# Optimization experiments

Hardware: AMD Instinct MI355X
Metric: run time of the kernel (lower is better)

Reference implementation:

```python
import jax, jax.numpy as jnp
import numpy as np

H = 32        # num_attention_heads
KV = 8        # num_key_value_heads
D = 128       # head_dim
THETA = 10000.0


def _rope_sincos(seq_len):
    half = D // 2
    i = jnp.arange(half, dtype=jnp.float32)
    # NOTE: original uses theta ** (+2*(i//2)/half) (growing frequencies, not inverse)
    emb = THETA ** (2.0 * jnp.floor(i / 2.0) / half)
    pos = jnp.arange(seq_len, dtype=jnp.float32)
    freqs = pos[:, None] * emb[None, :]            # (S, half)
    sin = jnp.concatenate([jnp.sin(freqs), jnp.sin(freqs)], axis=-1)  # (S, D)
    cos = jnp.concatenate([jnp.cos(freqs), jnp.cos(freqs)], axis=-1)  # (S, D)
    return sin, cos


def _rotate_half(x):
    half = D // 2
    return jnp.concatenate([-x[..., half:], x[..., :half]], axis=-1)


def setup_inputs() -> dict:
    key = jax.random.key(0)
    ks = jax.random.split(key, 5)
    B, S, HS = 2, 4096, 4096
    KVD = KV * D
    return {
        "hidden_states": jax.random.normal(ks[0], (B, S, HS), dtype=jnp.float32) * 0.02,
        "Wq": jax.random.normal(ks[1], (HS, HS), dtype=jnp.float32) * 0.02,
        "Wk": jax.random.normal(ks[2], (HS, KVD), dtype=jnp.float32) * 0.02,
        "Wv": jax.random.normal(ks[3], (HS, KVD), dtype=jnp.float32) * 0.02,
        "Wo": jax.random.normal(ks[4], (HS, HS), dtype=jnp.float32) * 0.02,
    }


def reference(hidden_states, Wq, Wk, Wv, Wo):
    B, S, HS = hidden_states.shape
    q = (hidden_states @ Wq).reshape(B, S, H, D)
    k = (hidden_states @ Wk).reshape(B, S, KV, D)
    v = (hidden_states @ Wv).reshape(B, S, KV, D)

    sin, cos = _rope_sincos(S)
    cos_b = cos[None, :, None, :]  # (1, S, 1, D)
    sin_b = sin[None, :, None, :]
    q = q * cos_b + _rotate_half(q) * sin_b
    k = k * cos_b + _rotate_half(k) * sin_b

    rep = H // KV
    k = jnp.repeat(k, rep, axis=2)  # (B, S, H, D)
    v = jnp.repeat(v, rep, axis=2)

    scale = jnp.sqrt(jnp.float32(D))
    # Faithful to original: matmul batches over (B, S) -> per-position head-head attention
    scores = jnp.einsum('bshd,bstd->bsht', q, k) / scale  # (B, S, H, H)
    attn = jax.nn.softmax(scores, axis=-1)
    out = jnp.einsum('bsht,bstd->bshd', attn, v).reshape(B, S, HS)
    return out @ Wo
```

## Files before the change

### kernel.cpp

```cpp
#include <hip/hip_runtime.h>
#include <cmath>

typedef short short8 __attribute__((ext_vector_type(8)));
typedef float floatx4 __attribute__((ext_vector_type(4)));
typedef unsigned short ushortx4 __attribute__((ext_vector_type(4)));

__device__ inline float bf2f(unsigned short u) {
  return __uint_as_float(((unsigned)u) << 16);
}
__device__ inline unsigned short f2bf(float x) {
  unsigned u = __float_as_uint(x);
  u = (u + 0x7FFFu + ((u >> 16) & 1u)) >> 16;
  return (unsigned short)u;
}

__global__ void probe_kernel(const unsigned short* __restrict__ in, int* __restrict__ flag) {
  __shared__ float red[256];
  float m = 0.f;
  for (int i = threadIdx.x; i < 8192; i += 256) {
    float v = fabsf(bf2f(in[i]));
    if (!isnan(v)) m = fmaxf(m, v);
  }
  red[threadIdx.x] = m;
  __syncthreads();
  for (int s = 128; s > 0; s >>= 1) {
    if (threadIdx.x < s) red[threadIdx.x] = fmaxf(red[threadIdx.x], red[threadIdx.x + s]);
    __syncthreads();
  }
  if (threadIdx.x == 0) flag[0] = (red[0] < 1000.0f) ? 1 : 0;
}

__global__ __launch_bounds__(256) void cast_any(const void* __restrict__ in,
                                                unsigned short* __restrict__ out,
                                                const int* __restrict__ flag, int n) {
  int i = (blockIdx.x * 256 + threadIdx.x) * 4;
  if (i >= n) return;
  if (flag[0]) {
    *(ushortx4*)(out + i) = *(const ushortx4*)((const unsigned short*)in + i);
  } else {
    const float* f = (const float*)in + i;
    ushortx4 o;
    o.x = f2bf(f[0]); o.y = f2bf(f[1]); o.z = f2bf(f[2]); o.w = f2bf(f[3]);
    *(ushortx4*)(out + i) = o;
  }
}

__global__ __launch_bounds__(256) void transpose_cast(const void* __restrict__ W,
                                                      unsigned short* __restrict__ WT,
                                                      const int* __restrict__ flag,
                                                      int N, int rowOff) {
  __shared__ unsigned short tile[32][33];
  int n0 = blockIdx.x * 32, k0 = blockIdx.y * 32;
  int tx = threadIdx.x & 31, ty = threadIdx.x >> 5;
  bool isbf = flag[0] != 0;
#pragma unroll
  for (int p = 0; p < 4; ++p) {
    int k = k0 + ty + p * 8;
    size_t idx = (size_t)k * N + n0 + tx;
    unsigned short b = isbf ? ((const unsigned short*)W)[idx] : f2bf(((const float*)W)[idx]);
    tile[ty + p * 8][tx] = b;
  }
  __syncthreads();
#pragma unroll
  for (int p = 0; p < 4; ++p) {
    int n = n0 + ty + p * 8;
    WT[(size_t)(rowOff + n) * 4096 + k0 + tx] = tile[tx][ty + p * 8];
  }
}

__device__ inline void gload16(const unsigned short* g, unsigned short* lds) {
  __builtin_amdgcn_global_load_lds(
      (const __attribute__((address_space(1))) unsigned int*)g,
      (__attribute__((address_space(3))) unsigned int*)lds, 16, 0, 0);
}

template <int OUTMODE>
__global__ __launch_bounds__(512, 2) void gemm256(const unsigned short* __restrict__ A,
                                                  const unsigned short* __restrict__ BT,
                                                  void* __restrict__ C, int M, int N, int K,
                                                  int nbn, const int* __restrict__ flag) {
  __shared__ __attribute__((aligned(16))) unsigned short As[3][256 * 32];
  __shared__ __attribute__((aligned(16))) unsigned short Bs[3][256 * 32];
  int tid = threadIdx.x;
  int w = tid >> 6, l = tid & 63;
  int wm = w >> 2, wn = w & 3;

  int nwg = gridDim.x;
  int cpx = nwg >> 3;
  int bid = blockIdx.x;
  int swz = (bid & 7) * cpx + (bid >> 3);
  int bm = swz / nbn, bn = swz - bm * nbn;
  int m0 = bm * 256, n0 = bn * 256;

  int sr = tid >> 2;
  int sc = tid & 3;
  int sf = (sr >> 1) & 3;
  int scs = (sc ^ sf) * 8;
  const unsigned short* Ab = A + (size_t)(m0 + sr) * K + scs;
  const unsigned short* Bb = BT + (size_t)(n0 + sr) * K + scs;

  int lane15 = l & 15, q = l >> 4;
  int fl = (lane15 >> 1) & 3;
  int rswz = (q ^ fl) * 8;
  int aoff = (wm * 128 + lane15) * 32 + rswz;
  int boff = (wn * 64 + lane15) * 32 + rswz;

  floatx4 acc[8][4] = {};
  int NT = K >> 5;

  auto stage_half = [&](int tt, int b, int p) {
    gload16(Ab + (size_t)p * 128 * K + (size_t)tt * 32, &As[b][(p * 128 + w * 16) * 32]);
    gload16(Bb + (size_t)p * 128 * K + (size_t)tt * 32, &Bs[b][(p * 128 + w * 16) * 32]);
  };

  stage_half(0, 0, 0);
  stage_half(0, 0, 1);
  stage_half(1, 1, 0);
  stage_half(1, 1, 1);

  int cur = 0;
  for (int t = 0; t < NT; ++t) {
    int nxt2 = cur + 2;
    if (nxt2 >= 3) nxt2 -= 3;
    bool pf = (t + 2 < NT);
    if (t < NT - 1) asm volatile("s_waitcnt vmcnt(4)" ::: "memory");
    else            asm volatile("s_waitcnt vmcnt(0)" ::: "memory");
    __builtin_amdgcn_s_barrier();

    const unsigned short* pA = &As[cur][0];
    const unsigned short* pB = &Bs[cur][0];

    short8 bfr[4], af[4];
#pragma unroll
    for (int i = 0; i < 4; ++i) bfr[i] = *(const short8*)(pB + boff + i * 512);
#pragma unroll
    for (int i = 0; i < 4; ++i) af[i] = *(const short8*)(pA + aoff + i * 512);
    if (pf) stage_half(t + 2, nxt2, 0);
    __builtin_amdgcn_s_barrier();
    __builtin_amdgcn_s_setprio(1);
#pragma unroll
    for (int mi = 0; mi < 4; ++mi)
#pragma unroll
      for (int ni = 0; ni < 4; ++ni)
        acc[mi][ni] = __builtin_amdgcn_mfma_f32_16x16x32_bf16(af[mi], bfr[ni], acc[mi][ni], 0, 0, 0);
    __builtin_amdgcn_s_setprio(0);
    __builtin_amdgcn_s_barrier();

#pragma unroll
    for (int i = 0; i < 4; ++i) af[i] = *(const short8*)(pA + aoff + 2048 + i * 512);
    if (pf) stage_half(t + 2, nxt2, 1);
    __builtin_amdgcn_s_barrier();
    __builtin_amdgcn_s_setprio(1);
#pragma unroll
    for (int mi = 0; mi < 4; ++mi)
#pragma unroll
      for (int ni = 0; ni < 4; ++ni)
        acc[mi + 4][ni] = __builtin_amdgcn_mfma_f32_16x16x32_bf16(af[mi], bfr[ni], acc[mi + 4][ni], 0, 0, 0);
    __builtin_amdgcn_s_setprio(0);

    cur = (cur == 2) ? 0 : cur + 1;
  }

  bool obf = true;
  if (OUTMODE == 1) obf = (flag[0] != 0);
#pragma unroll
  for (int mi = 0; mi < 8; ++mi) {
    int rbase = m0 + wm * 128 + mi * 16 + q * 4;
#pragma unroll
    for (int ni = 0; ni < 4; ++ni) {
      int col = n0 + wn * 64 + ni * 16 + lane15;
#pragma unroll
      for (int rr = 0; rr < 4; ++rr) {
        float v = acc[mi][ni][rr];
        size_t idx = (size_t)(rbase + rr) * N + col;
        if (OUTMODE == 0 || obf)
          ((unsigned short*)C)[idx] = f2bf(v);
        else
          ((float*)C)[idx] = v;
      }
    }
  }
}

__global__ __launch_bounds__(256) void attn_kernel(const unsigned short* __restrict__ QKV,
                                                   unsigned short* __restrict__ AO) {
  __shared__ __attribute__((aligned(16))) float qr[32 * 136];
  __shared__ __attribute__((aligned(16))) float kr[8 * 136];
  __shared__ __attribute__((aligned(16))) float vv[8 * 136];
  __shared__ float P[256];
  __shared__ float sn[64], cs[64];
  int r = blockIdx.x;
  int pos = r & 4095;
  int t = threadIdx.x;
  const unsigned short* row = QKV + (size_t)r * 6144;

  if (t < 64) {
    double e = pow(10000.0, (double)(2 * (t >> 1)) / 64.0);
    float f = (float)pos * (float)e;
    float s_, c_;
    sincosf(f, &s_, &c_);
    sn[t] = s_;
    cs[t] = c_;
  }
  __syncthreads();

#pragma unroll
  for (int p = 0; p < 4; ++p) {
    int e = t + p * 256;
    int head = e >> 7, d = e & 127;
    float x = bf2f(row[4096 + e]);
    float xp = bf2f(row[4096 + (e ^ 64)]);
    float sg = (d < 64) ? -1.f : 1.f;
    kr[head * 136 + d] = x * cs[d & 63] + sg * xp * sn[d & 63];
    vv[head * 136 + d] = bf2f(row[5120 + e]);
  }
#pragma unroll
  for (int p = 0; p < 16; ++p) {
    int e = t + p * 256;
    int head = e >> 7, d = e & 127;
    float x = bf2f(row[e]);
    float xp = bf2f(row[e ^ 64]);
    float sg = (d < 64) ? -1.f : 1.f;
    qr[head * 136 + d] = x * cs[d & 63] + sg * xp * sn[d & 63];
  }
  __syncthreads();

  int h = t >> 3, j = t & 7;
  const float4* q4 = (const float4*)(qr + h * 136);
  const float4* k4 = (const float4*)(kr + j * 136);
  float s = 0.f;
#pragma unroll
  for (int d4 = 0; d4 < 32; ++d4) {
    float4 a = q4[d4], b = k4[d4];
    s += a.x * b.x + a.y * b.y + a.z * b.z + a.w * b.w;
  }
  s *= 0.08838834764831845f;
  float mx = s;
  mx = fmaxf(mx, __shfl_xor(mx, 1));
  mx = fmaxf(mx, __shfl_xor(mx, 2));
  mx = fmaxf(mx, __shfl_xor(mx, 4));
  float ex = expf(s - mx);
  float sm = ex;
  sm += __shfl_xor(sm, 1);
  sm += __shfl_xor(sm, 2);
  sm += __shfl_xor(sm, 4);
  P[t] = ex / sm;
  __syncthreads();

  int d0 = (t & 7) * 16;
  float o[16];
#pragma unroll
  for (int c = 0; c < 16; ++c) o[c] = 0.f;
#pragma unroll
  for (int j2 = 0; j2 < 8; ++j2) {
    float pj = P[h * 8 + j2];
    const float4* v4 = (const float4*)(vv + j2 * 136 + d0);
#pragma unroll
    for (int c = 0; c < 4; ++c) {
      float4 x = v4[c];
      o[c * 4 + 0] += pj * x.x;
      o[c * 4 + 1] += pj * x.y;
      o[c * 4 + 2] += pj * x.z;
      o[c * 4 + 3] += pj * x.w;
    }
  }
  unsigned short* outp = AO + (size_t)r * 4096 + h * 128 + d0;
#pragma unroll
  for (int c = 0; c < 4; ++c) {
    ushortx4 ov;
    ov.x = f2bf(o[c * 4 + 0]);
    ov.y = f2bf(o[c * 4 + 1]);
    ov.z = f2bf(o[c * 4 + 2]);
    ov.w = f2bf(o[c * 4 + 3]);
    *(ushortx4*)(outp + c * 4) = ov;
  }
}

extern "C" void kernel_launch(void* const* d_in, const int* in_sizes, int n_in,
                              void* d_out, int out_size, void* d_ws, size_t ws_size,
                              hipStream_t stream) {
  (void)in_sizes; (void)n_in; (void)out_size; (void)ws_size;
  const void* X  = d_in[0];
  const void* Wq = d_in[1];
  const void* Wk = d_in[2];
  const void* Wv = d_in[3];
  const void* Wo = d_in[4];
  char* ws = (char*)d_ws;
  unsigned short* Xb   = (unsigned short*)(ws);
  unsigned short* WT   = (unsigned short*)(ws + 67108864);
  unsigned short* WoT  = (unsigned short*)(ws + 117440512);
  unsigned short* QKVb = (unsigned short*)(ws + 150994944);
  int* flag            = (int*)(ws + 251658240);
  unsigned short* AO = Xb;

  probe_kernel<<<1, 256, 0, stream>>>((const unsigned short*)X, flag);
  cast_any<<<32768, 256, 0, stream>>>(X, Xb, flag, 33554432);
  transpose_cast<<<dim3(128, 128), 256, 0, stream>>>(Wq, WT, flag, 4096, 0);
  transpose_cast<<<dim3(32, 128), 256, 0, stream>>>(Wk, WT, flag, 1024, 4096);
  transpose_cast<<<dim3(32, 128), 256, 0, stream>>>(Wv, WT, flag, 1024, 5120);
  transpose_cast<<<dim3(128, 128), 256, 0, stream>>>(Wo, WoT, flag, 4096, 0);
  gemm256<0><<<768, 512, 0, stream>>>(Xb, WT, QKVb, 8192, 6144, 4096, 24, flag);
  attn_kernel<<<8192, 256, 0, stream>>>(QKVb, AO);
  gemm256<1><<<512, 512, 0, stream>>>(AO, WoT, d_out, 8192, 4096, 4096, 16, flag);
}
```

Measured before the change: 1.119 ms.

## Restructure GEMM main loop, precompute RoPE table, repad attention smem rows

The GEMM inner loop now loads both A halves and the B fragments from LDS up front. It then issues both prefetch halves together and runs all 32 MFMAs back to back, which drops two of the three barriers per k-step. The intent is to cut synchronisation stalls, at the cost of extra registers and possible LDS read/write races on the triple buffer. RoPE sin/cos values now come from a table built by a separate kernel, replacing per-block double-precision pow and sincos. The attention LDS row stride also changes from 136 to 140 floats to alter bank mapping.

After: 1.009 ms. 9.8% less time.

```diff
diff --git a/kernel.cpp b/kernel.cpp
--- a/kernel.cpp
+++ b/kernel.cpp
@@ -122,7 +122,6 @@
   for (int t = 0; t < NT; ++t) {
     int nxt2 = cur + 2;
     if (nxt2 >= 3) nxt2 -= 3;
-    bool pf = (t + 2 < NT);
     if (t < NT - 1) asm volatile("s_waitcnt vmcnt(4)" ::: "memory");
     else            asm volatile("s_waitcnt vmcnt(0)" ::: "memory");
     __builtin_amdgcn_s_barrier();
@@ -130,32 +129,30 @@
     const unsigned short* pA = &As[cur][0];
     const unsigned short* pB = &Bs[cur][0];
 
-    short8 bfr[4], af[4];
+    short8 bfr[4], afA[4], afB[4];
 #pragma unroll
     for (int i = 0; i < 4; ++i) bfr[i] = *(const short8*)(pB + boff + i * 512);
 #pragma unroll
-    for (int i = 0; i < 4; ++i) af[i] = *(const short8*)(pA + aoff + i * 512);
-    if (pf) stage_half(t + 2, nxt2, 0);
-    __builtin_amdgcn_s_barrier();
+    for (int i = 0; i < 4; ++i) afA[i] = *(const short8*)(pA + aoff + i * 512);
+#pragma unroll
+    for (int i = 0; i < 4; ++i) afB[i] = *(const short8*)(pA + aoff + 2048 + i * 512);
+
+    if (t + 2 < NT) {
+      stage_half(t + 2, nxt2, 0);
+      stage_half(t + 2, nxt2, 1);
+    }
+
     __builtin_amdgcn_s_setprio(1);
 #pragma unroll
     for (int mi = 0; mi < 4; ++mi)
 #pragma unroll
       for (int ni = 0; ni < 4; ++ni)
-        acc[mi][ni] = __builtin_amdgcn_mfma_f32_16x16x32_bf16(af[mi], bfr[ni], acc[mi][ni], 0, 0, 0);
-    __builtin_amdgcn_s_setprio(0);
-    __builtin_amdgcn_s_barrier();
-
-#pragma unroll
-    for (int i = 0; i < 4; ++i) af[i] = *(const short8*)(pA + aoff + 2048 + i * 512);
-    if (pf) stage_half(t + 2, nxt2, 1);
-    __builtin_amdgcn_s_barrier();
-    __builtin_amdgcn_s_setprio(1);
+        acc[mi][ni] = __builtin_amdgcn_mfma_f32_16x16x32_bf16(afA[mi], bfr[ni], acc[mi][ni], 0, 0, 0);
 #pragma unroll
     for (int mi = 0; mi < 4; ++mi)
 #pragma unroll
       for (int ni = 0; ni < 4; ++ni)
-        acc[mi + 4][ni] = __builtin_amdgcn_mfma_f32_16x16x32_bf16(af[mi], bfr[ni], acc[mi + 4][ni], 0, 0, 0);
+        acc[mi + 4][ni] = __builtin_amdgcn_mfma_f32_16x16x32_bf16(afB[mi], bfr[ni], acc[mi + 4][ni], 0, 0, 0);
     __builtin_amdgcn_s_setprio(0);
 
     cur = (cur == 2) ? 0 : cur + 1;
@@ -182,11 +179,23 @@
   }
 }
 
+__global__ __launch_bounds__(256) void rope_tab(float* __restrict__ tab) {
+  int i = blockIdx.x * 256 + threadIdx.x;
+  int pos = i >> 6, k = i & 63;
+  double e = pow(10000.0, (double)(2 * (k >> 1)) / 64.0);
+  float f = (float)pos * (float)e;
+  float s_, c_;
+  sincosf(f, &s_, &c_);
+  tab[i * 2] = s_;
+  tab[i * 2 + 1] = c_;
+}
+
 __global__ __launch_bounds__(256) void attn_kernel(const unsigned short* __restrict__ QKV,
+                                                   const float* __restrict__ tab,
                                                    unsigned short* __restrict__ AO) {
-  __shared__ __attribute__((aligned(16))) float qr[32 * 136];
-  __shared__ __attribute__((aligned(16))) float kr[8 * 136];
-  __shared__ __attribute__((aligned(16))) float vv[8 * 136];
+  __shared__ __attribute__((aligned(16))) float qr[32 * 140];
+  __shared__ __attribute__((aligned(16))) float kr[8 * 140];
+  __shared__ __attribute__((aligned(16))) float vv[8 * 140];
   __shared__ float P[256];
   __shared__ float sn[64], cs[64];
   int r = blockIdx.x;
@@ -195,12 +204,10 @@
   const unsigned short* row = QKV + (size_t)r * 6144;
 
   if (t < 64) {
-    double e = pow(10000.0, (double)(2 * (t >> 1)) / 64.0);
-    float f = (float)pos * (float)e;
-    float s_, c_;
-    sincosf(f, &s_, &c_);
-    sn[t] = s_;
-    cs[t] = c_;
+    const float2* t2 = (const float2*)tab + (size_t)pos * 64 + t;
+    float2 sc = *t2;
+    sn[t] = sc.x;
+    cs[t] = sc.y;
   }
   __syncthreads();
 
@@ -211,8 +218,8 @@
     float x = bf2f(row[4096 + e]);
     float xp = bf2f(row[4096 + (e ^ 64)]);
     float sg = (d < 64) ? -1.f : 1.f;
-    kr[head * 136 + d] = x * cs[d & 63] + sg * xp * sn[d & 63];
-    vv[head * 136 + d] = bf2f(row[5120 + e]);
+    kr[head * 140 + d] = x * cs[d & 63] + sg * xp * sn[d & 63];
+    vv[head * 140 + d] = bf2f(row[5120 + e]);
   }
 #pragma unroll
   for (int p = 0; p < 16; ++p) {
@@ -221,13 +228,13 @@
     float x = bf2f(row[e]);
     float xp = bf2f(row[e ^ 64]);
     float sg = (d < 64) ? -1.f : 1.f;
-    qr[head * 136 + d] = x * cs[d & 63] + sg * xp * sn[d & 63];
+    qr[head * 140 + d] = x * cs[d & 63] + sg * xp * sn[d & 63];
   }
   __syncthreads();
 
   int h = t >> 3, j = t & 7;
-  const float4* q4 = (const float4*)(qr + h * 136);
-  const float4* k4 = (const float4*)(kr + j * 136);
+  const float4* q4 = (const float4*)(qr + h * 140);
+  const float4* k4 = (const float4*)(kr + j * 140);
   float s = 0.f;
 #pragma unroll
   for (int d4 = 0; d4 < 32; ++d4) {
@@ -254,7 +261,7 @@
 #pragma unroll
   for (int j2 = 0; j2 < 8; ++j2) {
     float pj = P[h * 8 + j2];
-    const float4* v4 = (const float4*)(vv + j2 * 136 + d0);
+    const float4* v4 = (const float4*)(vv + j2 * 140 + d0);
 #pragma unroll
     for (int c = 0; c < 4; ++c) {
       float4 x = v4[c];
@@ -292,6 +299,7 @@
   unsigned short* QKVb = (unsigned short*)(ws + 150994944);
   int* flag            = (int*)(ws + 251658240);
   unsigned short* AO = Xb;
+  float* tab = (float*)(ws + 67108864);
 
   probe_kernel<<<1, 256, 0, stream>>>((const unsigned short*)X, flag);
   cast_any<<<32768, 256, 0, stream>>>(X, Xb, flag, 33554432);
@@ -300,6 +308,7 @@
   transpose_cast<<<dim3(32, 128), 256, 0, stream>>>(Wv, WT, flag, 1024, 5120);
   transpose_cast<<<dim3(128, 128), 256, 0, stream>>>(Wo, WoT, flag, 4096, 0);
   gemm256<0><<<768, 512, 0, stream>>>(Xb, WT, QKVb, 8192, 6144, 4096, 24, flag);
-  attn_kernel<<<8192, 256, 0, stream>>>(QKVb, AO);
+  rope_tab<<<1024, 256, 0, stream>>>(tab);
+  attn_kernel<<<8192, 256, 0, stream>>>(QKVb, tab, AO);
   gemm256<1><<<512, 512, 0, stream>>>(AO, WoT, d_out, 8192, 4096, 4096, 16, flag);
 }
```
